# Kernel tuning notes

Hardware: AMD Instinct MI355X
Metric: run time of the kernel (lower is better)

## Reference

```python
import jax, jax.numpy as jnp
import numpy as np

H = 64      # hidden width of each MLP
M_STEPS = 64   # SDE steps (m)
N_SIM = 2048   # Monte-Carlo paths (n)
D = 128        # number of options (data_size)


def _mlp4(x, W1, b1, W2, b2, W3, b3):
    # x: [n, d, 4]; weights stacked over the 4 networks on axis 0 (k)
    h = jax.nn.relu(jnp.einsum('ndf,kfh->kndh', x, W1) + b1[:, None, None, :])
    h = jax.nn.relu(jnp.einsum('kndh,khg->kndg', h, W2) + b2[:, None, None, :])
    o = jnp.einsum('kndg,kgo->kndo', h, W3) + b3[:, None, None, :]
    return jnp.tanh(o)  # [4, n, d, 1]


def setup_inputs() -> dict:
    key = jax.random.key(0)
    ks = jax.random.split(key, 12)
    S0 = jax.random.uniform(ks[0], (D,), jnp.float32, 50.0, 150.0)
    K = jax.random.uniform(ks[1], (D,), jnp.float32, 50.0, 150.0)
    T = jax.random.uniform(ks[2], (D,), jnp.float32, 0.25, 2.0)
    rf = jnp.array([0.03], jnp.float32)
    V0 = jnp.array([0.04], jnp.float32)
    rho = jnp.array([-0.5], jnp.float32)
    Z1 = jax.random.normal(ks[3], (M_STEPS, N_SIM, D), jnp.float32)
    Z2raw = jax.random.normal(ks[4], (M_STEPS, N_SIM, D), jnp.float32)
    # 4 MLPs, layers [4, H, H, 1]
    W1 = jax.random.normal(ks[5], (4, 4, H), jnp.float32) / jnp.sqrt(4.0)
    b1 = jnp.zeros((4, H), jnp.float32)
    W2 = jax.random.normal(ks[6], (4, H, H), jnp.float32) / jnp.sqrt(float(H))
    b2 = jnp.zeros((4, H), jnp.float32)
    W3 = jax.random.normal(ks[7], (4, H, 1), jnp.float32) / jnp.sqrt(float(H))
    b3 = jnp.zeros((4, 1), jnp.float32)
    return {"S0": S0, "K": K, "T": T, "rf": rf, "V0": V0, "rho": rho,
            "Z1": Z1, "Z2raw": Z2raw,
            "W1": W1, "b1": b1, "W2": W2, "b2": b2, "W3": W3, "b3": b3}


def reference(S0, K, T, rf, V0, rho, Z1, Z2raw, W1, b1, W2, b2, W3, b3):
    m, n, d = Z1.shape
    dt = (T / m)[None, :, None]          # [1, d, 1]
    sdt = jnp.sqrt(dt)
    rho_s = rho[0]
    rf_s = rf[0]
    S = jnp.broadcast_to(S0[None, :, None], (n, d, 1))
    V = jnp.broadcast_to(V0[0], (n, d, 1))

    def step(carry, xs):
        S, V = carry
        j, z1, z2r = xs                    # z1, z2r: [n, d]
        z2 = rho_s * z1 + jnp.sqrt(1.0 - rho_s ** 2) * z2r
        feat = jnp.concatenate([
            S, V,
            jnp.broadcast_to(rf_s, S.shape),
            jnp.broadcast_to(dt * j, S.shape),
        ], axis=2)                          # [n, d, 4]
        N1, N2, N3, N4 = _mlp4(feat, W1, b1, W2, b2, W3, b3)
        Vn = V * (1.0 + N3 * dt + N4 * sdt * z2[..., None])
        Sn = S * (1.0 + N1 * dt + N2 * sdt * z1[..., None])
        return (Sn, Vn), None

    js = jnp.arange(m, dtype=jnp.float32)
    (S, V), _ = jax.lax.scan(step, (S, V), (js, Z1, Z2raw))
    S = S[..., 0]                            # [n, d]
    payoff = jnp.maximum(S - K[None, :], 0.0)
    P_pred = jnp.sum(jnp.exp(-rf_s * T)[None, :] * payoff, axis=0) / n
    return P_pred
```

## Files before the change

kernel.cpp:

```cpp
#include <hip/hip_runtime.h>
#include <math.h>

#define D_OPT   128
#define N_SIM   2048
#define M_STEPS 64
#define HID     64


typedef _Float16 f16x8 __attribute__((ext_vector_type(8)));
typedef _Float16 f16x4 __attribute__((ext_vector_type(4)));
typedef _Float16 f16x2 __attribute__((ext_vector_type(2)));
typedef float    f32x4 __attribute__((ext_vector_type(4)));
typedef unsigned int u32;
typedef u32 u32x2 __attribute__((ext_vector_type(2)));
typedef u32 u32x4 __attribute__((ext_vector_type(4)));

__device__ __forceinline__ u32 pk2u(float a, float b) {
#if __has_builtin(__builtin_amdgcn_cvt_pkrtz)
    return __builtin_bit_cast(u32, __builtin_amdgcn_cvt_pkrtz(a, b));
#else
    f16x2 p; p[0] = (_Float16)a; p[1] = (_Float16)b;
    return __builtin_bit_cast(u32, p);
#endif
}

__device__ __forceinline__ u32 pk_relu_cvt(float a, float b) {
    f16x2 p = __builtin_bit_cast(f16x2, pk2u(a, b));
    const f16x2 z = { (_Float16)0.0f, (_Float16)0.0f };
#if __has_builtin(__builtin_elementwise_max)
    p = __builtin_elementwise_max(p, z);
#else
    p[0] = p[0] > z[0] ? p[0] : z[0];
    p[1] = p[1] > z[1] ? p[1] : z[1];
#endif
    return __builtin_bit_cast(u32, p);
}

__global__ __launch_bounds__(256, 4) void nsde_kernel(
    const float* __restrict__ S0p, const float* __restrict__ Kp,
    const float* __restrict__ Tp,  const float* __restrict__ rfp,
    const float* __restrict__ V0p, const float* __restrict__ rhop,
    const float* __restrict__ Z1,  const float* __restrict__ Z2r,
    const float* __restrict__ W1,  const float* __restrict__ B1,
    const float* __restrict__ W2,  const float* __restrict__ B2,
    const float* __restrict__ W3,  const float* __restrict__ B3,
    float* __restrict__ out)
{
    __shared__ float nvp[2][4][128];
    __shared__ u32x2 pkx[4][128];

    const int tid  = threadIdx.x;
    const int wave = tid >> 6;
    const int lane = tid & 63;
    const int q    = lane >> 4;
    const int mA   = lane & 15;
    const float rf = rfp[0];

    const float* w1g = W1 + wave * 256;
    const float* b1g = B1 + wave * 64;
    const float* w2g = W2 + wave * 4096;
    const float* b2g = B2 + wave * 64;
    const float* w3g = W3 + wave * 64;

    f16x4 A1[4];
    #pragma unroll
    for (int t = 0; t < 4; ++t) {
        f16x4 a = { (_Float16)0.0f, (_Float16)0.0f, (_Float16)0.0f, (_Float16)0.0f };
        if (q == 0) {
            const int h = t * 16 + mA;
            a[0] = (_Float16)w1g[0 * 64 + h];
            a[1] = (_Float16)w1g[1 * 64 + h];
            a[2] = (_Float16)w1g[3 * 64 + h];
            a[3] = (_Float16)fmaf(rf, w1g[2 * 64 + h], b1g[h]);
        }
        A1[t] = a;
    }

    f16x8 A2[4][2];
    #pragma unroll
    for (int gt = 0; gt < 4; ++gt)
        #pragma unroll
        for (int kt = 0; kt < 2; ++kt) {
            f16x8 a;
            #pragma unroll
            for (int j = 0; j < 8; ++j) {
                const int h1 = (2 * kt + (j >> 2)) * 16 + 4 * q + (j & 3);
                a[j] = (_Float16)w2g[h1 * 64 + gt * 16 + mA];
            }
            A2[gt][kt] = a;
        }

    f16x8 A3[2];
    #pragma unroll
    for (int kt = 0; kt < 2; ++kt) {
        f16x8 a;
        #pragma unroll
        for (int j = 0; j < 8; ++j) a[j] = (_Float16)0.0f;
        if (mA == 0) {
            #pragma unroll
            for (int j = 0; j < 8; ++j) {
                const int g = (2 * kt + (j >> 2)) * 16 + 4 * q + (j & 3);
                a[j] = (_Float16)w3g[g];
            }
        }
        A3[kt] = a;
    }

    f32x4 cinit2[4];
    #pragma unroll
    for (int t = 0; t < 4; ++t)
        #pragma unroll
        for (int r = 0; r < 4; ++r)
            cinit2[t][r] = b2g[t * 16 + 4 * q + r];
    const f32x4 zc = { 0.0f, 0.0f, 0.0f, 0.0f };

    const float b3n0 = B3[0], b3n1 = B3[1], b3n2 = B3[2], b3n3 = B3[3];

    const int ebase = blockIdx.x * 128;
    const int dA_ = (ebase + lane) & (D_OPT - 1);
    const int dB_ = (ebase + 64 + lane) & (D_OPT - 1);
    const float dtA  = Tp[dA_] * (1.0f / (float)M_STEPS);
    const float dtB  = Tp[dB_] * (1.0f / (float)M_STEPS);
    const float sdtA = sqrtf(dtA);
    const float sdtB = sqrtf(dtB);

    float SregA = S0p[dA_], SregB = S0p[dB_];
    float VregA = V0p[0],   VregB = V0p[0];
    {
        u32x2 pk0;
        pk0[0] = pk2u(SregA, VregA);
        pk0[1] = pk2u(0.0f, 1.0f);
        pkx[wave][lane] = pk0;
        u32x2 pk1;
        pk1[0] = pk2u(SregB, VregB);
        pk1[1] = pk2u(0.0f, 1.0f);
        pkx[wave][64 + lane] = pk1;
    }

    const float rho   = rhop[0];
    const float rho_c = sqrtf(1.0f - rho * rho);
    const size_t estep = (size_t)N_SIM * D_OPT;
    const float* z1p = Z1  + (size_t)ebase + (size_t)lane;
    const float* z2p = Z2r + (size_t)ebase + (size_t)lane;

    float z1cA = z1p[0], z1cB = z1p[64];
    float z2cA = z2p[0], z2cB = z2p[64];
    z1p += estep; z2p += estep;

    #pragma unroll 1
    for (int s = 0; s < M_STEPS; ++s) {
        const float z1nA = z1p[0], z1nB = z1p[64];
        const float z2nA = z2p[0], z2nB = z2p[64];
        const size_t adv = (s < M_STEPS - 2) ? estep : (size_t)0;
        z1p += adv; z2p += adv;

        #pragma unroll 2
        for (int mt = 0; mt < 8; ++mt) {
            const u32x2 pksv = pkx[wave][mt * 16 + mA];
            const f16x4 B1f = __builtin_bit_cast(f16x4, pksv);

            u32x4 b2u[2];
            #pragma unroll
            for (int t = 0; t < 4; ++t) {
                const f32x4 acc = __builtin_amdgcn_mfma_f32_16x16x16f16(
                                      A1[t], B1f, zc, 0, 0, 0);
                b2u[t >> 1][(t & 1) * 2 + 0] = pk_relu_cvt(acc[0], acc[1]);
                b2u[t >> 1][(t & 1) * 2 + 1] = pk_relu_cvt(acc[2], acc[3]);
            }
            const f16x8 B2f0 = __builtin_bit_cast(f16x8, b2u[0]);
            const f16x8 B2f1 = __builtin_bit_cast(f16x8, b2u[1]);

            u32x4 b3u[2];
            #pragma unroll
            for (int gt = 0; gt < 4; ++gt) {
                f32x4 acc = __builtin_amdgcn_mfma_f32_16x16x32_f16(
                                A2[gt][0], B2f0, cinit2[gt], 0, 0, 0);
                acc = __builtin_amdgcn_mfma_f32_16x16x32_f16(
                                A2[gt][1], B2f1, acc, 0, 0, 0);
                b3u[gt >> 1][(gt & 1) * 2 + 0] = pk_relu_cvt(acc[0], acc[1]);
                b3u[gt >> 1][(gt & 1) * 2 + 1] = pk_relu_cvt(acc[2], acc[3]);
            }

            f32x4 acc3 = __builtin_amdgcn_mfma_f32_16x16x32_f16(
                             A3[0], __builtin_bit_cast(f16x8, b3u[0]), zc, 0, 0, 0);
            acc3 = __builtin_amdgcn_mfma_f32_16x16x32_f16(
                             A3[1], __builtin_bit_cast(f16x8, b3u[1]), acc3, 0, 0, 0);

            if (q == 0)
                nvp[s & 1][wave][mt * 16 + mA] = acc3[0];
        }

        __builtin_amdgcn_sched_barrier(0);
        asm volatile("s_waitcnt lgkmcnt(0)\n\ts_barrier" ::: "memory");
        __builtin_amdgcn_sched_barrier(0);

        {
            const float o0 = nvp[s & 1][0][lane] + b3n0;
            const float o1 = nvp[s & 1][1][lane] + b3n1;
            const float o2 = nvp[s & 1][2][lane] + b3n2;
            const float o3 = nvp[s & 1][3][lane] + b3n3;
            const float e0 = __expf(2.0f * o0);
            const float e1 = __expf(2.0f * o1);
            const float e2 = __expf(2.0f * o2);
            const float e3 = __expf(2.0f * o3);
            const float N0 = 1.0f - 2.0f / (e0 + 1.0f);
            const float N1 = 1.0f - 2.0f / (e1 + 1.0f);
            const float N2 = 1.0f - 2.0f / (e2 + 1.0f);
            const float N3 = 1.0f - 2.0f / (e3 + 1.0f);
            const float z2 = fmaf(rho, z1cA, rho_c * z2cA);
            const float fS = fmaf(N1 * sdtA, z1cA, N0 * dtA);
            const float fV = fmaf(N3 * sdtA, z2, N2 * dtA);
            SregA = fmaf(SregA, fS, SregA);
            VregA = fmaf(VregA, fV, VregA);
            u32x2 pkn;
            pkn[0] = pk2u(SregA, VregA);
            pkn[1] = pk2u(dtA * (float)(s + 1), 1.0f);
            pkx[wave][lane] = pkn;
            z1cA = z1nA; z2cA = z2nA;
        }
        {
            const float o0 = nvp[s & 1][0][64 + lane] + b3n0;
            const float o1 = nvp[s & 1][1][64 + lane] + b3n1;
            const float o2 = nvp[s & 1][2][64 + lane] + b3n2;
            const float o3 = nvp[s & 1][3][64 + lane] + b3n3;
            const float e0 = __expf(2.0f * o0);
            const float e1 = __expf(2.0f * o1);
            const float e2 = __expf(2.0f * o2);
            const float e3 = __expf(2.0f * o3);
            const float N0 = 1.0f - 2.0f / (e0 + 1.0f);
            const float N1 = 1.0f - 2.0f / (e1 + 1.0f);
            const float N2 = 1.0f - 2.0f / (e2 + 1.0f);
            const float N3 = 1.0f - 2.0f / (e3 + 1.0f);
            const float z2 = fmaf(rho, z1cB, rho_c * z2cB);
            const float fS = fmaf(N1 * sdtB, z1cB, N0 * dtB);
            const float fV = fmaf(N3 * sdtB, z2, N2 * dtB);
            SregB = fmaf(SregB, fS, SregB);
            VregB = fmaf(VregB, fV, VregB);
            u32x2 pkn;
            pkn[0] = pk2u(SregB, VregB);
            pkn[1] = pk2u(dtB * (float)(s + 1), 1.0f);
            pkx[wave][64 + lane] = pkn;
            z1cB = z1nB; z2cB = z2nB;
        }
    }

    if (wave == 0) {
        const float TdA = dtA * (float)M_STEPS;
        const float pA  = fmaxf(SregA - Kp[dA_], 0.0f);
        atomicAdd(&out[dA_], __expf(-rf * TdA) * pA * (1.0f / (float)N_SIM));
        const float TdB = dtB * (float)M_STEPS;
        const float pB  = fmaxf(SregB - Kp[dB_], 0.0f);
        atomicAdd(&out[dB_], __expf(-rf * TdB) * pB * (1.0f / (float)N_SIM));
    }
}

extern "C" void kernel_launch(void* const* d_in, const int* in_sizes, int n_in,
                              void* d_out, int out_size, void* d_ws, size_t ws_size,
                              hipStream_t stream)
{
    const float* S0  = (const float*)d_in[0];
    const float* K   = (const float*)d_in[1];
    const float* T   = (const float*)d_in[2];
    const float* rf  = (const float*)d_in[3];
    const float* V0  = (const float*)d_in[4];
    const float* rho = (const float*)d_in[5];
    const float* Z1  = (const float*)d_in[6];
    const float* Z2r = (const float*)d_in[7];
    const float* W1  = (const float*)d_in[8];
    const float* B1  = (const float*)d_in[9];
    const float* W2  = (const float*)d_in[10];
    const float* B2  = (const float*)d_in[11];
    const float* W3  = (const float*)d_in[12];
    const float* B3  = (const float*)d_in[13];
    float* out = (float*)d_out;

    hipMemsetAsync(out, 0, (size_t)out_size * sizeof(float), stream);

    const int total = N_SIM * D_OPT;
    const int grid  = total / 128;
    nsde_kernel<<<grid, 256, 0, stream>>>(S0, K, T, rf, V0, rho, Z1, Z2r,
                                          W1, B1, W2, B2, W3, B3, out);
}
```

Before: 815.0 us.

## Ping-pong two path halves so MLP matmuls overlap the SDE update

Splits the 128 paths per block into two independent halves, A and B, each with its own LDS buffers. The MFMA MLP for one half now runs while the scalar tanh/exp update for the other half is in flight, with a barrier between phases. The goal is to hide the VALU/transcendental update latency behind matrix-core work instead of running them back to back. This doubles the number of barriers per step and adds a prologue LADDER before the loop.

```diff
diff --git a/kernel.cpp b/kernel.cpp
--- a/kernel.cpp
+++ b/kernel.cpp
@@ -36,6 +36,73 @@
     return __builtin_bit_cast(u32, p);
 }
 
+#define LADDER(PKXW, NVPW)                                                    \
+  do {                                                                        \
+    _Pragma("unroll 2")                                                       \
+    for (int mt = 0; mt < 4; ++mt) {                                          \
+      const u32x2 pksv = (PKXW)[mt * 16 + mA];                                \
+      const f16x4 B1f = __builtin_bit_cast(f16x4, pksv);                      \
+      u32x4 b2u[2];                                                           \
+      _Pragma("unroll")                                                       \
+      for (int t = 0; t < 4; ++t) {                                           \
+        const f32x4 acc = __builtin_amdgcn_mfma_f32_16x16x16f16(              \
+            A1[t], B1f, zc, 0, 0, 0);                                         \
+        b2u[t >> 1][(t & 1) * 2 + 0] = pk_relu_cvt(acc[0], acc[1]);           \
+        b2u[t >> 1][(t & 1) * 2 + 1] = pk_relu_cvt(acc[2], acc[3]);           \
+      }                                                                       \
+      const f16x8 B2f0 = __builtin_bit_cast(f16x8, b2u[0]);                   \
+      const f16x8 B2f1 = __builtin_bit_cast(f16x8, b2u[1]);                   \
+      u32x4 b3u[2];                                                           \
+      _Pragma("unroll")                                                       \
+      for (int gt = 0; gt < 4; ++gt) {                                        \
+        f32x4 acc = __builtin_amdgcn_mfma_f32_16x16x32_f16(                   \
+            A2[gt][0], B2f0, cinit2[gt], 0, 0, 0);                            \
+        acc = __builtin_amdgcn_mfma_f32_16x16x32_f16(                         \
+            A2[gt][1], B2f1, acc, 0, 0, 0);                                   \
+        b3u[gt >> 1][(gt & 1) * 2 + 0] = pk_relu_cvt(acc[0], acc[1]);         \
+        b3u[gt >> 1][(gt & 1) * 2 + 1] = pk_relu_cvt(acc[2], acc[3]);         \
+      }                                                                       \
+      f32x4 acc3 = __builtin_amdgcn_mfma_f32_16x16x32_f16(                    \
+          A3[0], __builtin_bit_cast(f16x8, b3u[0]), zc, 0, 0, 0);             \
+      acc3 = __builtin_amdgcn_mfma_f32_16x16x32_f16(                          \
+          A3[1], __builtin_bit_cast(f16x8, b3u[1]), acc3, 0, 0, 0);           \
+      if (q == 0) (NVPW)[mt * 16 + mA] = acc3[0];                             \
+    }                                                                         \
+  } while (0)
+
+#define UPDATE(NVPX, Sr, Vr, z1c, z2c, z1n, z2n, dtx, sdtx, PKXW, snext)      \
+  do {                                                                        \
+    const float o0 = (NVPX)[0][lane] + b3n0;                                  \
+    const float o1 = (NVPX)[1][lane] + b3n1;                                  \
+    const float o2 = (NVPX)[2][lane] + b3n2;                                  \
+    const float o3 = (NVPX)[3][lane] + b3n3;                                  \
+    const float e0 = __expf(2.0f * o0);                                       \
+    const float e1 = __expf(2.0f * o1);                                       \
+    const float e2 = __expf(2.0f * o2);                                       \
+    const float e3 = __expf(2.0f * o3);                                       \
+    const float N0 = 1.0f - 2.0f / (e0 + 1.0f);                               \
+    const float N1 = 1.0f - 2.0f / (e1 + 1.0f);                               \
+    const float N2 = 1.0f - 2.0f / (e2 + 1.0f);                               \
+    const float N3 = 1.0f - 2.0f / (e3 + 1.0f);                               \
+    const float zz2 = fmaf(rho, z1c, rho_c * z2c);                            \
+    const float fS = fmaf(N1 * sdtx, z1c, N0 * dtx);                          \
+    const float fV = fmaf(N3 * sdtx, zz2, N2 * dtx);                          \
+    Sr = fmaf(Sr, fS, Sr);                                                    \
+    Vr = fmaf(Vr, fV, Vr);                                                    \
+    u32x2 pkn;                                                                \
+    pkn[0] = pk2u(Sr, Vr);                                                    \
+    pkn[1] = pk2u(dtx * (float)(snext), 1.0f);                                \
+    (PKXW)[lane] = pkn;                                                       \
+    z1c = z1n; z2c = z2n;                                                     \
+  } while (0)
+
+#define LBAR()                                                                \
+  do {                                                                        \
+    __builtin_amdgcn_sched_barrier(0);                                        \
+    asm volatile("s_waitcnt lgkmcnt(0)\n\ts_barrier" ::: "memory");           \
+    __builtin_amdgcn_sched_barrier(0);                                        \
+  } while (0)
+
 __global__ __launch_bounds__(256, 4) void nsde_kernel(
     const float* __restrict__ S0p, const float* __restrict__ Kp,
     const float* __restrict__ Tp,  const float* __restrict__ rfp,
@@ -46,8 +113,8 @@
     const float* __restrict__ W3,  const float* __restrict__ B3,
     float* __restrict__ out)
 {
-    __shared__ float nvp[2][4][128];
-    __shared__ u32x2 pkx[4][128];
+    __shared__ float nvpA[4][64], nvpB[4][64];
+    __shared__ u32x2 pkxA[4][64], pkxB[4][64];
 
     const int tid  = threadIdx.x;
     const int wave = tid >> 6;
@@ -130,11 +197,11 @@
         u32x2 pk0;
         pk0[0] = pk2u(SregA, VregA);
         pk0[1] = pk2u(0.0f, 1.0f);
-        pkx[wave][lane] = pk0;
+        pkxA[wave][lane] = pk0;
         u32x2 pk1;
         pk1[0] = pk2u(SregB, VregB);
         pk1[1] = pk2u(0.0f, 1.0f);
-        pkx[wave][64 + lane] = pk1;
+        pkxB[wave][lane] = pk1;
     }
 
     const float rho   = rhop[0];
@@ -146,6 +213,10 @@
     float z1cA = z1p[0], z1cB = z1p[64];
     float z2cA = z2p[0], z2cB = z2p[64];
     z1p += estep; z2p += estep;
+
+    __syncthreads();
+    LADDER(pkxA[wave], nvpA[wave]);
+    LBAR();
 
     #pragma unroll 1
     for (int s = 0; s < M_STEPS; ++s) {
@@ -154,94 +225,16 @@
         const size_t adv = (s < M_STEPS - 2) ? estep : (size_t)0;
         z1p += adv; z2p += adv;
 
-        #pragma unroll 2
-        for (int mt = 0; mt < 8; ++mt) {
-            const u32x2 pksv = pkx[wave][mt * 16 + mA];
-            const f16x4 B1f = __builtin_bit_cast(f16x4, pksv);
-
-            u32x4 b2u[2];
-            #pragma unroll
-            for (int t = 0; t < 4; ++t) {
-                const f32x4 acc = __builtin_amdgcn_mfma_f32_16x16x16f16(
-                                      A1[t], B1f, zc, 0, 0, 0);
-                b2u[t >> 1][(t & 1) * 2 + 0] = pk_relu_cvt(acc[0], acc[1]);
-                b2u[t >> 1][(t & 1) * 2 + 1] = pk_relu_cvt(acc[2], acc[3]);
-            }
-            const f16x8 B2f0 = __builtin_bit_cast(f16x8, b2u[0]);
-            const f16x8 B2f1 = __builtin_bit_cast(f16x8, b2u[1]);
-
-            u32x4 b3u[2];
-            #pragma unroll
-            for (int gt = 0; gt < 4; ++gt) {
-                f32x4 acc = __builtin_amdgcn_mfma_f32_16x16x32_f16(
-                                A2[gt][0], B2f0, cinit2[gt], 0, 0, 0);
-                acc = __builtin_amdgcn_mfma_f32_16x16x32_f16(
-                                A2[gt][1], B2f1, acc, 0, 0, 0);
-                b3u[gt >> 1][(gt & 1) * 2 + 0] = pk_relu_cvt(acc[0], acc[1]);
-                b3u[gt >> 1][(gt & 1) * 2 + 1] = pk_relu_cvt(acc[2], acc[3]);
-            }
-
-            f32x4 acc3 = __builtin_amdgcn_mfma_f32_16x16x32_f16(
-                             A3[0], __builtin_bit_cast(f16x8, b3u[0]), zc, 0, 0, 0);
-            acc3 = __builtin_amdgcn_mfma_f32_16x16x32_f16(
-                             A3[1], __builtin_bit_cast(f16x8, b3u[1]), acc3, 0, 0, 0);
-
-            if (q == 0)
-                nvp[s & 1][wave][mt * 16 + mA] = acc3[0];
-        }
-
-        __builtin_amdgcn_sched_barrier(0);
-        asm volatile("s_waitcnt lgkmcnt(0)\n\ts_barrier" ::: "memory");
-        __builtin_amdgcn_sched_barrier(0);
-
-        {
-            const float o0 = nvp[s & 1][0][lane] + b3n0;
-            const float o1 = nvp[s & 1][1][lane] + b3n1;
-            const float o2 = nvp[s & 1][2][lane] + b3n2;
-            const float o3 = nvp[s & 1][3][lane] + b3n3;
-            const float e0 = __expf(2.0f * o0);
-            const float e1 = __expf(2.0f * o1);
-            const float e2 = __expf(2.0f * o2);
-            const float e3 = __expf(2.0f * o3);
-            const float N0 = 1.0f - 2.0f / (e0 + 1.0f);
-            const float N1 = 1.0f - 2.0f / (e1 + 1.0f);
-            const float N2 = 1.0f - 2.0f / (e2 + 1.0f);
-            const float N3 = 1.0f - 2.0f / (e3 + 1.0f);
-            const float z2 = fmaf(rho, z1cA, rho_c * z2cA);
-            const float fS = fmaf(N1 * sdtA, z1cA, N0 * dtA);
-            const float fV = fmaf(N3 * sdtA, z2, N2 * dtA);
-            SregA = fmaf(SregA, fS, SregA);
-            VregA = fmaf(VregA, fV, VregA);
-            u32x2 pkn;
-            pkn[0] = pk2u(SregA, VregA);
-            pkn[1] = pk2u(dtA * (float)(s + 1), 1.0f);
-            pkx[wave][lane] = pkn;
-            z1cA = z1nA; z2cA = z2nA;
-        }
-        {
-            const float o0 = nvp[s & 1][0][64 + lane] + b3n0;
-            const float o1 = nvp[s & 1][1][64 + lane] + b3n1;
-            const float o2 = nvp[s & 1][2][64 + lane] + b3n2;
-            const float o3 = nvp[s & 1][3][64 + lane] + b3n3;
-            const float e0 = __expf(2.0f * o0);
-            const float e1 = __expf(2.0f * o1);
-            const float e2 = __expf(2.0f * o2);
-            const float e3 = __expf(2.0f * o3);
-            const float N0 = 1.0f - 2.0f / (e0 + 1.0f);
-            const float N1 = 1.0f - 2.0f / (e1 + 1.0f);
-            const float N2 = 1.0f - 2.0f / (e2 + 1.0f);
-            const float N3 = 1.0f - 2.0f / (e3 + 1.0f);
-            const float z2 = fmaf(rho, z1cB, rho_c * z2cB);
-            const float fS = fmaf(N1 * sdtB, z1cB, N0 * dtB);
-            const float fV = fmaf(N3 * sdtB, z2, N2 * dtB);
-            SregB = fmaf(SregB, fS, SregB);
-            VregB = fmaf(VregB, fV, VregB);
-            u32x2 pkn;
-            pkn[0] = pk2u(SregB, VregB);
-            pkn[1] = pk2u(dtB * (float)(s + 1), 1.0f);
-            pkx[wave][64 + lane] = pkn;
-            z1cB = z1nB; z2cB = z2nB;
-        }
+        LADDER(pkxB[wave], nvpB[wave]);
+        UPDATE(nvpA, SregA, VregA, z1cA, z2cA, z1nA, z2nA, dtA, sdtA,
+               pkxA[wave], s + 1);
+        LBAR();
+
+        if (s + 1 < M_STEPS)
+            LADDER(pkxA[wave], nvpA[wave]);
+        UPDATE(nvpB, SregB, VregB, z1cB, z2cB, z1nB, z2nB, dtB, sdtB,
+               pkxB[wave], s + 1);
+        LBAR();
     }
 
     if (wave == 0) {
```

New measurement: 819.4 us. No clear change (+0.5%).
